# Kernel tuning notes

Measured on AMD Instinct MI355X. Metric: run time of the kernel, lower is better.

## Reference

```python
import jax, jax.numpy as jnp
import numpy as np

BN_EPS = 1e-5
LN_EPS = 1e-5

N_NODES = 50000
N_EDGES = 800000
D_IN = 128
D_HID = 512


def _batchnorm(h, gamma, beta):
    # training-mode BatchNorm1d: biased variance over the node/batch dim
    m = jnp.mean(h, axis=0)
    v = jnp.mean(jnp.square(h - m), axis=0)
    return (h - m) * jax.lax.rsqrt(v + BN_EPS) * gamma + beta


def setup_inputs() -> dict:
    key = jax.random.key(0)
    ks = jax.random.split(key, 8)
    x = jax.random.normal(ks[0], (N_NODES, D_IN), dtype=jnp.float32)
    edge_index = jax.random.randint(ks[1], (2, N_EDGES), 0, N_NODES, dtype=jnp.int64)
    s1 = 1.0 / np.sqrt(D_IN)
    s2 = 1.0 / np.sqrt(D_HID)
    W1 = jax.random.uniform(ks[2], (D_IN, D_HID), jnp.float32, -s1, s1)
    b1 = jax.random.uniform(ks[3], (D_HID,), jnp.float32, -s1, s1)
    W2 = jax.random.uniform(ks[4], (D_HID, D_IN), jnp.float32, -s2, s2)
    b2 = jax.random.uniform(ks[5], (D_IN,), jnp.float32, -s2, s2)
    return {
        "x": x,
        "edge_index": edge_index,
        "W1": W1, "b1": b1,
        "bn1_g": jnp.ones((D_HID,), jnp.float32), "bn1_b": jnp.zeros((D_HID,), jnp.float32),
        "W2": W2, "b2": b2,
        "bn2_g": jnp.ones((D_IN,), jnp.float32), "bn2_b": jnp.zeros((D_IN,), jnp.float32),
        "ln_g": jnp.ones((D_IN,), jnp.float32), "ln_b": jnp.zeros((D_IN,), jnp.float32),
    }


def reference(x, edge_index, W1, b1, bn1_g, bn1_b, W2, b2, bn2_g, bn2_b, ln_g, ln_b):
    n = x.shape[0]
    src = edge_index[0]
    dst = edge_index[1]
    # GIN aggregation: sum of neighbor (source) features at each destination node
    agg = jax.ops.segment_sum(x[src], dst, num_segments=n)  # [N, D_IN]
    h = x + agg  # (1 + eps) * x + agg, eps = 0
    # MLP: Linear -> BN -> ReLU -> Linear -> BN -> ReLU (final activation)
    h = jax.nn.relu(_batchnorm(h @ W1 + b1, bn1_g, bn1_b))  # [N, D_HID]
    h = jax.nn.relu(_batchnorm(h @ W2 + b2, bn2_g, bn2_b))  # [N, D_IN]
    # residual + LayerNorm (dropout p=0 -> identity)
    out = h + x
    m = jnp.mean(out, axis=-1, keepdims=True)
    v = jnp.mean(jnp.square(out - m), axis=-1, keepdims=True)
    out = (out - m) * jax.lax.rsqrt(v + LN_EPS) * ln_g + ln_b
    return out
```

## Files before the change

kernel.cpp:

```cpp
#include <hip/hip_runtime.h>
#include <stdint.h>

#define N_NODES 50000
#define N_EDGES 800000
#define D_IN    128
#define D_HID   512
#define NPAD    50048
#define NTILES  391
#define SCAN_NB 196
#define G_TILES 782
#define G_BLOCKS 256
#define H1_FULL_NEED 64797440LL
#define FILL_CH 2048
#define FILL_SUB ((N_EDGES + FILL_CH - 1) / FILL_CH)

typedef __attribute__((ext_vector_type(8))) short short8;
typedef __attribute__((ext_vector_type(4))) float f32x4;

__device__ __forceinline__ float bf2f(unsigned short u) {
    union { unsigned int i; float f; } v; v.i = ((unsigned int)u) << 16; return v.f;
}
__device__ __forceinline__ unsigned short f2bf(float f) {
    union { float f; unsigned int i; } v; v.f = f;
    unsigned int r = v.i + 0x7fffu + ((v.i >> 16) & 1u);
    return (unsigned short)(r >> 16);
}
__device__ __forceinline__ float loadP(const void* p, long i, int isf) {
    return isf ? ((const float*)p)[i] : bf2f(((const unsigned short*)p)[i]);
}

__global__ void k_init(const void* __restrict__ x, const int* __restrict__ ei,
                       float* __restrict__ stats, int* __restrict__ counts,
                       int* __restrict__ flags) {
    int t = threadIdx.x;
    if (blockIdx.x < 201) {
        int i = blockIdx.x * 256 + t;
        if (i < 1408) stats[i] = 0.f;
        else if (i < 1408 + N_NODES) counts[i - 1408] = 0;
    } else {
        __shared__ int sh[2];
        if (t == 0) { sh[0] = 0; sh[1] = 1; }
        __syncthreads();
        const unsigned short* xu = (const unsigned short*)x;
        for (int i = t; i < 8192; i += 256)
            if (((xu[i] >> 7) & 0xFF) == 0xFF) sh[0] = 1;
        for (int k = t; k < 64; k += 256)
            if (ei[2 * k + 1] != 0) sh[1] = 0;
        __syncthreads();
        if (t == 0) { flags[0] = sh[0]; flags[1] = sh[1]; }
    }
}

__global__ __launch_bounds__(256) void k_prep(const void* __restrict__ W1, const void* __restrict__ W2,
                                              unsigned short* __restrict__ w1t, unsigned short* __restrict__ w2t,
                                              const int* __restrict__ ei, int* __restrict__ counts,
                                              const int* __restrict__ flags) {
    int isf = flags[0];
    if (blockIdx.x < 512) {
        int idx = blockIdx.x * 256 + threadIdx.x;
        if (idx < D_IN * D_HID) {
            int n = idx >> 7, k = idx & 127;
            int src = k * D_HID + n;
            w1t[idx] = isf ? f2bf(((const float*)W1)[src])
                           : ((const unsigned short*)W1)[src];
        } else {
            int j = idx - D_IN * D_HID;
            int n = j >> 9, k = j & 511;
            int src = k * D_IN + n;
            w2t[j] = isf ? f2bf(((const float*)W2)[src])
                         : ((const unsigned short*)W2)[src];
        }
    } else {
        int i64 = flags[1];
        int bid = blockIdx.x - 512;
        int gid = bid & 7;
        int sub = bid >> 3;
        int lo = gid * (N_NODES / 8), hi = lo + (N_NODES / 8);
        int base = sub * FILL_CH + threadIdx.x;
#pragma unroll
        for (int i = 0; i < 8; i++) {
            int e = base + i * 256;
            if (e < N_EDGES) {
                int d = i64 ? ei[2 * N_EDGES + 2 * e] : ei[N_EDGES + e];
                d = min(max(d, 0), N_NODES - 1);
                if (d >= lo && d < hi) atomicAdd(&counts[d], 1);
            }
        }
    }
}

__global__ __launch_bounds__(256) void k_scan_block(const int* __restrict__ counts,
                                                    int* __restrict__ rowptr,
                                                    int* __restrict__ partials) {
    __shared__ int a[256], b[256];
    int t = threadIdx.x;
    int idx = blockIdx.x * 256 + t;
    int c = (idx < N_NODES) ? counts[idx] : 0;
    a[t] = c;
    __syncthreads();
    int* src = a; int* dst = b;
    for (int off = 1; off < 256; off <<= 1) {
        dst[t] = src[t] + ((t >= off) ? src[t - off] : 0);
        __syncthreads();
        int* tmp = src; src = dst; dst = tmp;
    }
    if (idx < N_NODES) rowptr[idx] = src[t] - c;
    if (t == 255) partials[blockIdx.x] = src[255];
}

__global__ __launch_bounds__(256) void k_scan_add(int* __restrict__ rowptr, int* __restrict__ cursor,
                                                  const int* __restrict__ partials) {
    __shared__ int red[256];
    int t = threadIdx.x, bid = blockIdx.x;
    red[t] = (t < SCAN_NB && t < bid) ? partials[t] : 0;
    __syncthreads();
#pragma unroll
    for (int off = 128; off > 0; off >>= 1) {
        if (t < off) red[t] += red[t + off];
        __syncthreads();
    }
    int prefix = red[0];
    int idx = bid * 256 + t;
    if (idx < N_NODES) {
        int v = rowptr[idx] + prefix;
        rowptr[idx] = v;
        cursor[idx] = v;
    } else if (idx == N_NODES) {
        rowptr[N_NODES] = N_EDGES;
    }
}

__global__ __launch_bounds__(256) void k_fill(const int* __restrict__ ei, int* __restrict__ cursor,
                                              int* __restrict__ bucket, const int* __restrict__ flags) {
    int i64 = flags[1];
    int gid = blockIdx.x & 7;
    int sub = blockIdx.x >> 3;
    int lo = gid * (N_NODES / 8), hi = lo + (N_NODES / 8);
    int base = sub * FILL_CH + threadIdx.x;
#pragma unroll
    for (int i = 0; i < 8; i++) {
        int e = base + i * 256;
        if (e < N_EDGES) {
            int d = i64 ? ei[2 * N_EDGES + 2 * e] : ei[N_EDGES + e];
            d = min(max(d, 0), N_NODES - 1);
            if (d >= lo && d < hi) {
                int s = i64 ? ei[2 * e] : ei[e];
                s = min(max(s, 0), N_NODES - 1);
                int pos = atomicAdd(&cursor[d], 1);
                bucket[pos] = s;
            }
        }
    }
}

__global__ __launch_bounds__(256) void k_gather(const int* __restrict__ rowptr,
                                                const int* __restrict__ bucket,
                                                const void* __restrict__ x,
                                                unsigned short* __restrict__ agg,
                                                const int* __restrict__ flags) {
    int isf = flags[0];
    int w = threadIdx.x >> 6, lane = threadIdx.x & 63;
    int row = blockIdx.x * 4 + w;
    float a0 = 0.f, a1 = 0.f;
    if (row < N_NODES) {
        int beg = rowptr[row], end = rowptr[row + 1];
        if (isf) {
            const float* xf = (const float*)x;
            float2 v = *(const float2*)(xf + (size_t)row * D_IN + lane * 2);
            a0 = v.x; a1 = v.y;
            int j = beg;
            for (; j + 8 <= end; j += 8) {
                float2 n0 = *(const float2*)(xf + (size_t)bucket[j] * D_IN + lane * 2);
                float2 n1 = *(const float2*)(xf + (size_t)bucket[j + 1] * D_IN + lane * 2);
                float2 n2 = *(const float2*)(xf + (size_t)bucket[j + 2] * D_IN + lane * 2);
                float2 n3 = *(const float2*)(xf + (size_t)bucket[j + 3] * D_IN + lane * 2);
                float2 n4 = *(const float2*)(xf + (size_t)bucket[j + 4] * D_IN + lane * 2);
                float2 n5 = *(const float2*)(xf + (size_t)bucket[j + 5] * D_IN + lane * 2);
                float2 n6 = *(const float2*)(xf + (size_t)bucket[j + 6] * D_IN + lane * 2);
                float2 n7 = *(const float2*)(xf + (size_t)bucket[j + 7] * D_IN + lane * 2);
                a0 += ((n0.x + n1.x) + (n2.x + n3.x)) + ((n4.x + n5.x) + (n6.x + n7.x));
                a1 += ((n0.y + n1.y) + (n2.y + n3.y)) + ((n4.y + n5.y) + (n6.y + n7.y));
            }
            for (; j + 4 <= end; j += 4) {
                float2 n0 = *(const float2*)(xf + (size_t)bucket[j] * D_IN + lane * 2);
                float2 n1 = *(const float2*)(xf + (size_t)bucket[j + 1] * D_IN + lane * 2);
                float2 n2 = *(const float2*)(xf + (size_t)bucket[j + 2] * D_IN + lane * 2);
                float2 n3 = *(const float2*)(xf + (size_t)bucket[j + 3] * D_IN + lane * 2);
                a0 += (n0.x + n1.x) + (n2.x + n3.x);
                a1 += (n0.y + n1.y) + (n2.y + n3.y);
            }
            for (; j < end; j++) {
                float2 n = *(const float2*)(xf + (size_t)bucket[j] * D_IN + lane * 2);
                a0 += n.x; a1 += n.y;
            }
        } else {
            const unsigned int* xu = (const unsigned int*)x;
            unsigned int u = xu[(size_t)row * 64 + lane];
            a0 = bf2f(u & 0xffff); a1 = bf2f(u >> 16);
            int j = beg;
            for (; j + 8 <= end; j += 8) {
                unsigned int u0 = xu[(size_t)bucket[j] * 64 + lane];
                unsigned int u1 = xu[(size_t)bucket[j + 1] * 64 + lane];
                unsigned int u2 = xu[(size_t)bucket[j + 2] * 64 + lane];
                unsigned int u3 = xu[(size_t)bucket[j + 3] * 64 + lane];
                unsigned int u4 = xu[(size_t)bucket[j + 4] * 64 + lane];
                unsigned int u5 = xu[(size_t)bucket[j + 5] * 64 + lane];
                unsigned int u6 = xu[(size_t)bucket[j + 6] * 64 + lane];
                unsigned int u7 = xu[(size_t)bucket[j + 7] * 64 + lane];
                a0 += ((bf2f(u0 & 0xffff) + bf2f(u1 & 0xffff)) + (bf2f(u2 & 0xffff) + bf2f(u3 & 0xffff)))
                    + ((bf2f(u4 & 0xffff) + bf2f(u5 & 0xffff)) + (bf2f(u6 & 0xffff) + bf2f(u7 & 0xffff)));
                a1 += ((bf2f(u0 >> 16) + bf2f(u1 >> 16)) + (bf2f(u2 >> 16) + bf2f(u3 >> 16)))
                    + ((bf2f(u4 >> 16) + bf2f(u5 >> 16)) + (bf2f(u6 >> 16) + bf2f(u7 >> 16)));
            }
            for (; j + 4 <= end; j += 4) {
                unsigned int u0 = xu[(size_t)bucket[j] * 64 + lane];
                unsigned int u1 = xu[(size_t)bucket[j + 1] * 64 + lane];
                unsigned int u2 = xu[(size_t)bucket[j + 2] * 64 + lane];
                unsigned int u3 = xu[(size_t)bucket[j + 3] * 64 + lane];
                a0 += (bf2f(u0 & 0xffff) + bf2f(u1 & 0xffff)) + (bf2f(u2 & 0xffff) + bf2f(u3 & 0xffff));
                a1 += (bf2f(u0 >> 16) + bf2f(u1 >> 16)) + (bf2f(u2 >> 16) + bf2f(u3 >> 16));
            }
            for (; j < end; j++) {
                unsigned int n = xu[(size_t)bucket[j] * 64 + lane];
                a0 += bf2f(n & 0xffff); a1 += bf2f(n >> 16);
            }
        }
    }
    unsigned int o = (unsigned int)f2bf(a0) | ((unsigned int)f2bf(a1) << 16);
    ((unsigned int*)agg)[(size_t)row * 64 + lane] = o;
}

__global__ __launch_bounds__(256) void k_gram(const unsigned short* __restrict__ aggb,
                                              float* __restrict__ Gpart,
                                              float* __restrict__ colsum) {
    __shared__ unsigned short ldsT[128 * 64];
    int t = threadIdx.x;
    int wid = t >> 6, lane = t & 63;
    int wm = wid & 1, wn = wid >> 1;
    int quad = lane >> 4, l16 = lane & 15;
    f32x4 acc[4][4] = {};
    float cs = 0.f;
    int cscol = t & 127, cskh = t >> 7;
    for (int tile = blockIdx.x; tile < G_TILES; tile += G_BLOCKS) {
        __syncthreads();
        size_t rowbase = (size_t)tile * 64;
#pragma unroll
        for (int jj = 0; jj < 2; jj++) {
            int j = t + jj * 256;
            int c = j >> 5, rp = j & 31;
            uint4 v0 = *(const uint4*)(aggb + (rowbase + 2 * rp) * 128 + c * 8);
            uint4 v1 = *(const uint4*)(aggb + (rowbase + 2 * rp + 1) * 128 + c * 8);
            const unsigned short* p0 = (const unsigned short*)&v0;
            const unsigned short* p1 = (const unsigned short*)&v1;
            int k = 2 * rp, kc = k >> 3, ko = k & 7;
#pragma unroll
            for (int e = 0; e < 8; e++) {
                int col = c * 8 + e;
                *(unsigned int*)(ldsT + col * 64 + ((kc ^ (col & 7)) * 8) + ko) =
                    (unsigned int)p0[e] | ((unsigned int)p1[e] << 16);
            }
        }
        __syncthreads();
#pragma unroll
        for (int ksub = 0; ksub < 2; ksub++) {
            short8 fa[4], fb[4];
#pragma unroll
            for (int mt = 0; mt < 4; mt++) {
                int col = wm * 64 + mt * 16 + l16;
                fa[mt] = *(const short8*)(ldsT + col * 64 + (((ksub * 4 + quad) ^ (col & 7)) * 8));
            }
#pragma unroll
            for (int nt = 0; nt < 4; nt++) {
                int col = wn * 64 + nt * 16 + l16;
                fb[nt] = *(const short8*)(ldsT + col * 64 + (((ksub * 4 + quad) ^ (col & 7)) * 8));
            }
#pragma unroll
            for (int mt = 0; mt < 4; mt++)
#pragma unroll
                for (int nt = 0; nt < 4; nt++)
                    acc[mt][nt] = __builtin_amdgcn_mfma_f32_16x16x32_bf16(fa[mt], fb[nt], acc[mt][nt], 0, 0, 0);
        }
#pragma unroll
        for (int kc = 0; kc < 4; kc++) {
            short8 v = *(const short8*)(ldsT + cscol * 64 + (((cskh * 4 + kc) ^ (cscol & 7)) * 8));
#pragma unroll
            for (int e = 0; e < 8; e++) cs += bf2f((unsigned short)v[e]);
        }
    }
    float* gp = Gpart + (size_t)blockIdx.x * 16384;
#pragma unroll
    for (int mt = 0; mt < 4; mt++)
#pragma unroll
        for (int nt = 0; nt < 4; nt++) {
            int m = wm * 64 + mt * 16 + quad * 4;
            int n = wn * 64 + nt * 16 + l16;
#pragma unroll
            for (int rg = 0; rg < 4; rg++)
                gp[(m + rg) * 128 + n] = acc[mt][nt][rg];
        }
    atomicAdd(&colsum[cscol], cs);
}

__global__ void k_gred(const float* __restrict__ Gpart, float* __restrict__ G) {
    int i = blockIdx.x * 256 + threadIdx.x;
    float s = 0.f;
#pragma unroll 8
    for (int b = 0; b < G_BLOCKS; b++) s += Gpart[(size_t)b * 16384 + i];
    G[i] = s;
}

__global__ __launch_bounds__(256) void k_bn1(const float* __restrict__ G,
                                             const float* __restrict__ colsum,
                                             const unsigned short* __restrict__ w1t,
                                             const void* __restrict__ b1,
                                             float* __restrict__ sum1,
                                             float* __restrict__ sumsq1,
                                             const int* __restrict__ flags) {
    int isf = flags[0];
    __shared__ float wsh[4][128];
    int t = threadIdx.x, wid = t >> 6, lane = t & 63;
    int n = blockIdx.x * 4 + wid;
    unsigned int u = *(const unsigned int*)(w1t + (size_t)n * 128 + lane * 2);
    wsh[wid][lane * 2] = bf2f(u & 0xffff);
    wsh[wid][lane * 2 + 1] = bf2f(u >> 16);
    __syncthreads();
    const float* w = wsh[wid];
    const f32x4* g0 = (const f32x4*)(G + (size_t)lane * 128);
    const f32x4* g1 = (const f32x4*)(G + (size_t)(lane + 64) * 128);
    float t0 = 0.f, t1 = 0.f;
#pragma unroll 4
    for (int q4 = 0; q4 < 32; q4++) {
        f32x4 a = g0[q4], b = g1[q4];
        float w0 = w[q4 * 4], w1 = w[q4 * 4 + 1], w2 = w[q4 * 4 + 2], w3 = w[q4 * 4 + 3];
        t0 += a[0] * w0 + a[1] * w1 + a[2] * w2 + a[3] * w3;
        t1 += b[0] * w0 + b[1] * w1 + b[2] * w2 + b[3] * w3;
    }
    float sq = w[lane] * t0 + w[lane + 64] * t1;
    float s  = w[lane] * colsum[lane] + w[lane + 64] * colsum[lane + 64];
#pragma unroll
    for (int m = 1; m < 64; m <<= 1) {
        sq += __shfl_xor(sq, m, 64);
        s  += __shfl_xor(s, m, 64);
    }
    if (lane == 0) {
        float b = loadP(b1, n, isf);
        sum1[n]   = s + (float)N_NODES * b;
        sumsq1[n] = sq + 2.f * b * s + (float)N_NODES * b * b;
    }
}

__global__ __launch_bounds__(256, 2) void k_mlp1(const unsigned short* __restrict__ aggc,
                                                 const unsigned short* __restrict__ w1t,
                                                 const void* __restrict__ b1,
                                                 const void* __restrict__ g1,
                                                 const void* __restrict__ bb1,
                                                 const float* __restrict__ sum1,
                                                 const float* __restrict__ sumsq1,
                                                 unsigned short* __restrict__ h1c,
                                                 const int* __restrict__ flags) {
    __shared__ unsigned short bufA[128 * 128];
    __shared__ unsigned short bufW[128 * 128];
    int isf = flags[0];
    int t = threadIdx.x;
    int m0 = (blockIdx.x >> 2) * 128;
    int nb = blockIdx.x & 3;
    int r = t >> 1, half = t & 1;
    int wid = t >> 6, lane = t & 63;
    int wm = wid & 1, wn = wid >> 1;
    int quad = lane >> 4, l16 = lane & 15;
#pragma unroll
    for (int i = 0; i < 8; i++) {
        int chunk = half * 8 + i;
        int sw = ((chunk ^ (r & 15)) * 8);
        *(uint4*)(bufA + r * 128 + sw) = *(const uint4*)(aggc + (size_t)(m0 + r) * 128 + chunk * 8);
        *(uint4*)(bufW + r * 128 + sw) = *(const uint4*)(w1t + (size_t)(nb * 128 + r) * 128 + chunk * 8);
    }
    __syncthreads();
    f32x4 acc[4][4] = {};
#pragma unroll
    for (int ks = 0; ks < 4; ks++) {
        short8 af[4], bw[4];
#pragma unroll
        for (int mt = 0; mt < 4; mt++)
            af[mt] = *(const short8*)(bufA + (wm * 64 + mt * 16 + l16) * 128 + (((ks * 4 + quad) ^ l16) * 8));
#pragma unroll
        for (int nt = 0; nt < 4; nt++)
            bw[nt] = *(const short8*)(bufW + (wn * 64 + nt * 16 + l16) * 128 + (((ks * 4 + quad) ^ l16) * 8));
#pragma unroll
        for (int mt = 0; mt < 4; mt++)
#pragma unroll
            for (int nt = 0; nt < 4; nt++)
                acc[mt][nt] = __builtin_amdgcn_mfma_f32_16x16x32_bf16(af[mt], bw[nt], acc[mt][nt], 0, 0, 0);
    }
    __syncthreads();
#pragma unroll
    for (int nt = 0; nt < 4; nt++) {
        int nl = wn * 64 + nt * 16 + l16;
        int n1 = nb * 128 + nl;
        float mz = sum1[n1] * (1.f / N_NODES);
        float vz = sumsq1[n1] * (1.f / N_NODES) - mz * mz;
        float inv = rsqrtf(fmaxf(vz, 0.f) + 1e-5f);
        float A = loadP(g1, n1, isf) * inv;
        float C = loadP(bb1, n1, isf) - mz * A + loadP(b1, n1, isf) * A;
        int ccw = nl >> 3, cl = nl & 7;
#pragma unroll
        for (int mt = 0; mt < 4; mt++)
#pragma unroll
            for (int rg = 0; rg < 4; rg++) {
                int R = wm * 64 + mt * 16 + quad * 4 + rg;
                bufA[R * 128 + ((ccw ^ (R & 15)) * 8) + cl] = f2bf(fmaxf(acc[mt][nt][rg] * A + C, 0.f));
            }
    }
    __syncthreads();
#pragma unroll
    for (int i = 0; i < 8; i++) {
        int idx = t + i * 256;
        int rr = idx >> 4, chunk = idx & 15;
        *(uint4*)(h1c + (size_t)(m0 + rr) * D_HID + nb * 128 + chunk * 8) =
            *(const uint4*)(bufA + rr * 128 + ((chunk ^ (rr & 15)) * 8));
    }
}

__global__ __launch_bounds__(256, 2) void k_mlp1r(const unsigned short* __restrict__ aggb,
                                                  const unsigned short* __restrict__ w1t,
                                                  const void* __restrict__ b1,
                                                  unsigned short* __restrict__ h1,
                                                  float* __restrict__ sum1,
                                                  float* __restrict__ sumsq1,
                                                  const int* __restrict__ flags) {
    __shared__ unsigned short bufA[128 * 128];
    __shared__ unsigned short bufW[128 * 128];
    __shared__ float sred[256];
    int isf = flags[0];
    int t = threadIdx.x;
    int m0 = (blockIdx.x >> 2) * 128;
    int nb = blockIdx.x & 3;
    int r = t >> 1, half = t & 1;
    int wid = t >> 6, lane = t & 63;
    int wm = wid & 1, wn = wid >> 1;
    int quad = lane >> 4, l16 = lane & 15;
    sred[t] = 0.f;
#pragma unroll
    for (int i = 0; i < 8; i++) {
        int chunk = half * 8 + i;
        int sw = ((chunk ^ (r & 15)) * 8);
        *(uint4*)(bufA + r * 128 + sw) = *(const uint4*)(aggb + (size_t)(m0 + r) * 128 + chunk * 8);
        *(uint4*)(bufW + r * 128 + sw) = *(const uint4*)(w1t + (size_t)(nb * 128 + r) * 128 + chunk * 8);
    }
    __syncthreads();
    f32x4 acc[4][4] = {};
#pragma unroll
    for (int ks = 0; ks < 4; ks++) {
        short8 af[4], bw[4];
#pragma unroll
        for (int mt = 0; mt < 4; mt++)
            af[mt] = *(const short8*)(bufA + (wm * 64 + mt * 16 + l16) * 128 + (((ks * 4 + quad) ^ l16) * 8));
#pragma unroll
        for (int nt = 0; nt < 4; nt++)
            bw[nt] = *(const short8*)(bufW + (wn * 64 + nt * 16 + l16) * 128 + (((ks * 4 + quad) ^ l16) * 8));
#pragma unroll
        for (int mt = 0; mt < 4; mt++)
#pragma unroll
            for (int nt = 0; nt < 4; nt++)
                acc[mt][nt] = __builtin_amdgcn_mfma_f32_16x16x32_bf16(af[mt], bw[nt], acc[mt][nt], 0, 0, 0);
    }
    __syncthreads();
#pragma unroll
    for (int nt = 0; nt < 4; nt++) {
        int nl = wn * 64 + nt * 16 + l16;
        int n1 = nb * 128 + nl;
        float bias = loadP(b1, n1, isf);
        int ccw = nl >> 3, cl = nl & 7;
        float s = 0.f, ss = 0.f;
#pragma unroll
        for (int mt = 0; mt < 4; mt++)
#pragma unroll
            for (int rg = 0; rg < 4; rg++) {
                int R = wm * 64 + mt * 16 + quad * 4 + rg;
                float z = acc[mt][nt][rg] + bias;
                bufA[R * 128 + ((ccw ^ (R & 15)) * 8) + cl] = f2bf(z);
                if (m0 + R < N_NODES) { s += z; ss += z * z; }
            }
        s += __shfl_xor(s, 16, 64); ss += __shfl_xor(ss, 16, 64);
        s += __shfl_xor(s, 32, 64); ss += __shfl_xor(ss, 32, 64);
        if (quad == 0) { atomicAdd(&sred[nl], s); atomicAdd(&sred[128 + nl], ss); }
    }
    __syncthreads();
#pragma unroll
    for (int i = 0; i < 8; i++) {
        int idx = t + i * 256;
        int rr = idx >> 4, chunk = idx & 15;
        *(uint4*)(h1 + (size_t)(m0 + rr) * D_HID + nb * 128 + chunk * 8) =
            *(const uint4*)(bufA + rr * 128 + ((chunk ^ (rr & 15)) * 8));
    }
    if (t < 128)      atomicAdd(&sum1[nb * 128 + t], sred[t]);
    else              atomicAdd(&sumsq1[nb * 128 + (t - 128)], sred[t]);
}

__global__ __launch_bounds__(256, 3) void k_mlp2(const unsigned short* __restrict__ h1c,
                                                 const unsigned short* __restrict__ w2t,
                                                 const void* __restrict__ b2,
                                                 unsigned short* __restrict__ h2c,
                                                 float* __restrict__ sum2,
                                                 float* __restrict__ sumsq2,
                                                 const int* __restrict__ flags,
                                                 int roff) {
    __shared__ unsigned short bufA[64 * 128];
    __shared__ unsigned short bufW[128 * 128];
    __shared__ float sred[256];
    int isf = flags[0];
    int t = threadIdx.x;
    int m0 = blockIdx.x * 64;
    int rw = t >> 1, halfw = t & 1;
    int wid = t >> 6, lane = t & 63;
    int wm = wid & 1, wn = wid >> 1;
    int quad = lane >> 4, l16 = lane & 15;
    sred[t] = 0.f;
    f32x4 acc[2][4] = {};
    for (int kb = 0; kb < 4; kb++) {
        __syncthreads();
#pragma unroll
        for (int i = 0; i < 4; i++) {
            int idx = t + i * 256;
            int rr = idx >> 4, chunk = idx & 15;
            *(uint4*)(bufA + rr * 128 + ((chunk ^ (rr & 15)) * 8)) =
                *(const uint4*)(h1c + (size_t)(m0 + rr) * D_HID + kb * 128 + chunk * 8);
        }
#pragma unroll
        for (int i = 0; i < 8; i++) {
            int chunk = halfw * 8 + i;
            *(uint4*)(bufW + rw * 128 + ((chunk ^ (rw & 15)) * 8)) =
                *(const uint4*)(w2t + (size_t)rw * D_HID + kb * 128 + chunk * 8);
        }
        __syncthreads();
#pragma unroll
        for (int ks = 0; ks < 4; ks++) {
            short8 af[2], bw[4];
#pragma unroll
            for (int mt = 0; mt < 2; mt++)
                af[mt] = *(const short8*)(bufA + (wm * 32 + mt * 16 + l16) * 128 + (((ks * 4 + quad) ^ l16) * 8));
#pragma unroll
            for (int nt = 0; nt < 4; nt++)
                bw[nt] = *(const short8*)(bufW + (wn * 64 + nt * 16 + l16) * 128 + (((ks * 4 + quad) ^ l16) * 8));
#pragma unroll
            for (int mt = 0; mt < 2; mt++)
#pragma unroll
                for (int nt = 0; nt < 4; nt++)
                    acc[mt][nt] = __builtin_amdgcn_mfma_f32_16x16x32_bf16(af[mt], bw[nt], acc[mt][nt], 0, 0, 0);
        }
    }
    __syncthreads();
#pragma unroll
    for (int nt = 0; nt < 4; nt++) {
        int n = wn * 64 + nt * 16 + l16;
        float bias = loadP(b2, n, isf);
        float s = 0.f, ss = 0.f;
#pragma unroll
        for (int mt = 0; mt < 2; mt++) {
            int Rl = wm * 32 + mt * 16 + quad * 4;
#pragma unroll
            for (int rg = 0; rg < 4; rg++) {
                float z = acc[mt][nt][rg] + bias;
                bufW[(Rl + rg) * 128 + n] = f2bf(z);
                if (roff + m0 + Rl + rg < N_NODES) { s += z; ss += z * z; }
            }
        }
        s += __shfl_xor(s, 16, 64); ss += __shfl_xor(ss, 16, 64);
        s += __shfl_xor(s, 32, 64); ss += __shfl_xor(ss, 32, 64);
        if (quad == 0) { atomicAdd(&sred[n], s); atomicAdd(&sred[128 + n], ss); }
    }
    __syncthreads();
#pragma unroll
    for (int i = 0; i < 4; i++) {
        int idx = t + i * 256;
        int rr = idx >> 4, seg = idx & 15;
        *(uint4*)(h2c + (size_t)(m0 + rr) * D_IN + seg * 8) = *(const uint4*)(bufW + rr * 128 + seg * 8);
    }
    {
        int n = t & 127;
        if (t < 128) atomicAdd(&sum2[n], sred[n]);
        else         atomicAdd(&sumsq2[n], sred[128 + n]);
    }
}

__global__ __launch_bounds__(512, 4) void k_mlp2b(const unsigned short* __restrict__ h1,
                                                  const unsigned short* __restrict__ w2t,
                                                  const void* __restrict__ b2,
                                                  const void* __restrict__ g1,
                                                  const void* __restrict__ bb1,
                                                  const float* __restrict__ sum1,
                                                  const float* __restrict__ sumsq1,
                                                  unsigned short* __restrict__ h2,
                                                  float* __restrict__ sum2,
                                                  float* __restrict__ sumsq2,
                                                  const int* __restrict__ flags) {
    __shared__ unsigned short bufA[128 * 128];
    __shared__ unsigned short bufW[128 * 128];
    __shared__ float sred[256];
    __shared__ __align__(16) float bnA[512];
    __shared__ __align__(16) float bnC[512];
    int isf = flags[0];
    int t = threadIdx.x;
    int m0 = blockIdx.x * 128;
    int wid = t >> 6, lane = t & 63;
    int wm = wid & 3, wn = wid >> 2;
    int quad = lane >> 4, l16 = lane & 15;
    int chunkT = t & 15;
    if (t < 256) sred[t] = 0.f;
    if (t < 512) {
        float mz = sum1[t] * (1.f / N_NODES);
        float vz = sumsq1[t] * (1.f / N_NODES) - mz * mz;
        float inv = rsqrtf(fmaxf(vz, 0.f) + 1e-5f);
        float A = loadP(g1, t, isf) * inv;
        bnA[t] = A;
        bnC[t] = loadP(bb1, t, isf) - mz * A;
    }
    f32x4 acc[2][4] = {};
    for (int kb = 0; kb < 4; kb++) {
        __syncthreads();
        f32x4 A0 = *(const f32x4*)(bnA + kb * 128 + chunkT * 8);
        f32x4 A1 = *(const f32x4*)(bnA + kb * 128 + chunkT * 8 + 4);
        f32x4 C0 = *(const f32x4*)(bnC + kb * 128 + chunkT * 8);
        f32x4 C1 = *(const f32x4*)(bnC + kb * 128 + chunkT * 8 + 4);
#pragma unroll
        for (int i = 0; i < 4; i++) {
            int idx = t + i * 512;
            int rr = idx >> 4;
            uint4 v = *(const uint4*)(h1 + (size_t)(m0 + rr) * D_HID + kb * 128 + chunkT * 8);
            const unsigned short* pv = (const unsigned short*)&v;
            unsigned short o[8];
            o[0] = f2bf(fmaxf(bf2f(pv[0]) * A0[0] + C0[0], 0.f));
            o[1] = f2bf(fmaxf(bf2f(pv[1]) * A0[1] + C0[1], 0.f));
            o[2] = f2bf(fmaxf(bf2f(pv[2]) * A0[2] + C0[2], 0.f));
            o[3] = f2bf(fmaxf(bf2f(pv[3]) * A0[3] + C0[3], 0.f));
            o[4] = f2bf(fmaxf(bf2f(pv[4]) * A1[0] + C1[0], 0.f));
            o[5] = f2bf(fmaxf(bf2f(pv[5]) * A1[1] + C1[1], 0.f));
            o[6] = f2bf(fmaxf(bf2f(pv[6]) * A1[2] + C1[2], 0.f));
            o[7] = f2bf(fmaxf(bf2f(pv[7]) * A1[3] + C1[3], 0.f));
            *(uint4*)(bufA + rr * 128 + ((chunkT ^ (rr & 15)) * 8)) = *(const uint4*)o;
        }
#pragma unroll
        for (int i = 0; i < 4; i++) {
            int idx = t + i * 512;
            int rr = idx >> 4;
            *(uint4*)(bufW + rr * 128 + ((chunkT ^ (rr & 15)) * 8)) =
                *(const uint4*)(w2t + (size_t)rr * D_HID + kb * 128 + chunkT * 8);
        }
        __syncthreads();
#pragma unroll
        for (int ks = 0; ks < 4; ks++) {
            short8 af[2], bw[4];
#pragma unroll
            for (int mt = 0; mt < 2; mt++)
                af[mt] = *(const short8*)(bufA + (wm * 32 + mt * 16 + l16) * 128 + (((ks * 4 + quad) ^ l16) * 8));
#pragma unroll
            for (int nt = 0; nt < 4; nt++)
                bw[nt] = *(const short8*)(bufW + (wn * 64 + nt * 16 + l16) * 128 + (((ks * 4 + quad) ^ l16) * 8));
#pragma unroll
            for (int mt = 0; mt < 2; mt++)
#pragma unroll
                for (int nt = 0; nt < 4; nt++)
                    acc[mt][nt] = __builtin_amdgcn_mfma_f32_16x16x32_bf16(af[mt], bw[nt], acc[mt][nt], 0, 0, 0);
        }
    }
    __syncthreads();
#pragma unroll
    for (int nt = 0; nt < 4; nt++) {
        int n = wn * 64 + nt * 16 + l16;
        float bias = loadP(b2, n, isf);
        float s = 0.f, ss = 0.f;
#pragma unroll
        for (int mt = 0; mt < 2; mt++) {
            int Rl = wm * 32 + mt * 16 + quad * 4;
#pragma unroll
            for (int rg = 0; rg < 4; rg++) {
                float z = acc[mt][nt][rg] + bias;
                bufW[(Rl + rg) * 128 + n] = f2bf(z);
                if (m0 + Rl + rg < N_NODES) { s += z; ss += z * z; }
            }
        }
        s += __shfl_xor(s, 16, 64); ss += __shfl_xor(ss, 16, 64);
        s += __shfl_xor(s, 32, 64); ss += __shfl_xor(ss, 32, 64);
        if (quad == 0) { atomicAdd(&sred[n], s); atomicAdd(&sred[128 + n], ss); }
    }
    __syncthreads();
#pragma unroll
    for (int i = 0; i < 4; i++) {
        int idx = t + i * 512;
        int rr = idx >> 4, seg = idx & 15;
        *(uint4*)(h2 + (size_t)(m0 + rr) * D_IN + seg * 8) = *(const uint4*)(bufW + rr * 128 + seg * 8);
    }
    if (t < 256) {
        int n = t & 127;
        if (t < 128) atomicAdd(&sum2[n], sred[n]);
        else         atomicAdd(&sumsq2[n], sred[128 + n]);
    }
}

__global__ __launch_bounds__(256) void k_final(const unsigned short* __restrict__ h2,
                                               const void* __restrict__ x,
                                               const float* __restrict__ sum2,
                                               const float* __restrict__ sumsq2,
                                               const void* __restrict__ g2,
                                               const void* __restrict__ bb2,
                                               const void* __restrict__ lng,
                                               const void* __restrict__ lnb,
                                               void* __restrict__ out,
                                               const int* __restrict__ flags) {
    int isf = flags[0];
    __shared__ float a2s[D_IN], c2s[D_IN];
    int t = threadIdx.x;
    if (t < D_IN) {
        float m = sum2[t] * (1.f / N_NODES);
        float v = sumsq2[t] * (1.f / N_NODES) - m * m;
        float inv = rsqrtf(fmaxf(v, 0.f) + 1e-5f);
        float a = loadP(g2, t, isf) * inv;
        a2s[t] = a;
        c2s[t] = loadP(bb2, t, isf) - m * a;
    }
    __syncthreads();
    int w = t >> 6, lane = t & 63;
    int row = blockIdx.x * 4 + w;
    if (row >= N_NODES) return;
    size_t base = (size_t)row * D_IN;
    int c0 = lane * 2, c1 = lane * 2 + 1;
    unsigned int hu = ((const unsigned int*)h2)[base / 2 + lane];
    float x0, x1;
    if (isf) {
        float2 xv = *((const float2*)x + base / 2 + lane);
        x0 = xv.x; x1 = xv.y;
    } else {
        unsigned int xu = ((const unsigned int*)x)[base / 2 + lane];
        x0 = bf2f(xu & 0xffff); x1 = bf2f(xu >> 16);
    }
    float o0 = fmaxf(a2s[c0] * bf2f(hu & 0xffff) + c2s[c0], 0.f) + x0;
    float o1 = fmaxf(a2s[c1] * bf2f(hu >> 16) + c2s[c1], 0.f) + x1;
    float s = o0 + o1, ss = o0 * o0 + o1 * o1;
#pragma unroll
    for (int m = 1; m < 64; m <<= 1) {
        s += __shfl_xor(s, m, 64);
        ss += __shfl_xor(ss, m, 64);
    }
    float mean = s * (1.f / D_IN);
    float var = ss * (1.f / D_IN) - mean * mean;
    float inv = rsqrtf(fmaxf(var, 0.f) + 1e-5f);
    float r0 = (o0 - mean) * inv * loadP(lng, c0, isf) + loadP(lnb, c0, isf);
    float r1 = (o1 - mean) * inv * loadP(lng, c1, isf) + loadP(lnb, c1, isf);
    if (isf) {
        *((float2*)out + base / 2 + lane) = make_float2(r0, r1);
    } else {
        ((unsigned int*)out)[base / 2 + lane] = (unsigned int)f2bf(r0) | ((unsigned int)f2bf(r1) << 16);
    }
}

extern "C" void kernel_launch(void* const* d_in, const int* in_sizes, int n_in,
                              void* d_out, int out_size, void* d_ws, size_t ws_size,
                              hipStream_t stream) {
    const void* x    = d_in[0];
    const int*  ei   = (const int*)d_in[1];
    const void* W1   = d_in[2];
    const void* b1   = d_in[3];
    const void* bn1g = d_in[4];
    const void* bn1b = d_in[5];
    const void* W2   = d_in[6];
    const void* b2   = d_in[7];
    const void* bn2g = d_in[8];
    const void* bn2b = d_in[9];
    const void* lng  = d_in[10];
    const void* lnb  = d_in[11];

    char* ws = (char*)d_ws;
    float* stats   = (float*)ws;
    float* sum1    = stats;
    float* sumsq1  = stats + 512;
    float* sum2    = stats + 1024;
    float* sumsq2  = stats + 1152;
    float* colsum  = stats + 1280;
    int*   flags   = (int*)(ws + 5632);
    int*   partials= (int*)(ws + 5696);
    int*   rowptr  = (int*)(ws + 8192);
    int*   cursor  = (int*)(ws + 208256);
    unsigned short* w1t = (unsigned short*)(ws + 408320);
    unsigned short* w2t = (unsigned short*)(ws + 539392);
    float* G       = (float*)(ws + 670464);
    unsigned short* agg = (unsigned short*)(ws + 736000);
    unsigned short* h2  = agg;
    int*   bucket  = (int*)(ws + 13548288);
    float* Gpart   = (float*)(ws + 16748288);
    unsigned short* h1r = (unsigned short*)(ws + 13548288);

    k_init<<<202, 256, 0, stream>>>(x, ei, stats, cursor, flags);
    k_prep<<<512 + 8 * FILL_SUB, 256, 0, stream>>>(W1, W2, w1t, w2t, ei, cursor, flags);
    k_scan_block<<<SCAN_NB, 256, 0, stream>>>(cursor, rowptr, partials);
    k_scan_add<<<SCAN_NB, 256, 0, stream>>>(rowptr, cursor, partials);
    k_fill<<<8 * FILL_SUB, 256, 0, stream>>>(ei, cursor, bucket, flags);
    k_gather<<<NPAD / 4, 256, 0, stream>>>(rowptr, bucket, x, agg, flags);

    if ((long long)ws_size >= H1_FULL_NEED) {
        k_mlp1r<<<NTILES * 4, 256, 0, stream>>>(agg, w1t, b1, h1r, sum1, sumsq1, flags);
        k_mlp2b<<<NTILES, 512, 0, stream>>>(h1r, w2t, b2, bn1g, bn1b, sum1, sumsq1,
                                            h2, sum2, sumsq2, flags);
    } else {
        k_gram<<<G_BLOCKS, 256, 0, stream>>>(agg, Gpart, colsum);
        k_gred<<<64, 256, 0, stream>>>(Gpart, G);
        k_bn1<<<128, 256, 0, stream>>>(G, colsum, w1t, b1, sum1, sumsq1, flags);
        long long avail = (long long)ws_size - 13548288LL;
        int max_tiles = (avail > 0) ? (int)(avail / 131072LL) : 1;
        if (max_tiles < 1)  max_tiles = 1;
        if (max_tiles > NTILES) max_tiles = NTILES;
        int nch = (NTILES + max_tiles - 1) / max_tiles;
        int per = (NTILES + nch - 1) / nch;
        for (int done = 0; done < NTILES; done += per) {
            int nt = NTILES - done;
            if (nt > per) nt = per;
            const unsigned short* aggc = agg + (size_t)done * 128 * 128;
            unsigned short* h2c = h2 + (size_t)done * 128 * 128;
            k_mlp1<<<nt * 4, 256, 0, stream>>>(aggc, w1t, b1, bn1g, bn1b, sum1, sumsq1, h1r, flags);
            k_mlp2<<<nt * 2, 256, 0, stream>>>(h1r, w2t, b2, h2c, sum2, sumsq2, flags, done * 128);
        }
    }

    k_final<<<(N_NODES + 3) / 4, 256, 0, stream>>>(h2, x, sum2, sumsq2, bn2g, bn2b, lng, lnb, d_out, flags);
}
```

Measured before the change: 324.5 us.

## Fuse neighbor gather into first MLP GEMM kernel with LDS staging

Adds a kernel that performs the CSR neighbor aggregation for a 128-row tile directly into shared memory, then multiplies by W1 with MFMA and writes h1 plus BN1 statistics. This removes the separate gather launch and the global write/read of the aggregated tensor when the workspace is large enough. The trade-off is fewer, larger blocks doing the latency-bound gather serially per wave, and high LDS use that limits occupancy.

```diff
diff --git a/kernel.cpp b/kernel.cpp
--- a/kernel.cpp
+++ b/kernel.cpp
@@ -10,7 +10,8 @@
 #define SCAN_NB 196
 #define G_TILES 782
 #define G_BLOCKS 256
-#define H1_FULL_NEED 64797440LL
+#define H1_SEP_NEED   64797440LL
+#define H1_FUSED_NEED 67997440LL
 #define FILL_CH 2048
 #define FILL_SUB ((N_EDGES + FILL_CH - 1) / FILL_CH)
 
@@ -228,6 +229,162 @@
     }
     unsigned int o = (unsigned int)f2bf(a0) | ((unsigned int)f2bf(a1) << 16);
     ((unsigned int*)agg)[(size_t)row * 64 + lane] = o;
+}
+
+__global__ __launch_bounds__(512, 4) void k_gmlp1(const int* __restrict__ rowptr,
+                                                  const int* __restrict__ bucket,
+                                                  const void* __restrict__ x,
+                                                  const unsigned short* __restrict__ w1t,
+                                                  const void* __restrict__ b1,
+                                                  unsigned short* __restrict__ h1,
+                                                  float* __restrict__ sum1,
+                                                  float* __restrict__ sumsq1,
+                                                  const int* __restrict__ flags) {
+    __shared__ unsigned short bufA[128 * 128];
+    __shared__ unsigned short bufW[128 * 128];
+    __shared__ float sred[256];
+    int isf = flags[0];
+    int t = threadIdx.x;
+    int m0 = blockIdx.x * 128;
+    int w8 = t >> 6, lane = t & 63;
+    if (t < 256) sred[t] = 0.f;
+    for (int rl = 0; rl < 16; rl++) {
+        int r = w8 * 16 + rl;
+        int row = m0 + r;
+        float a0 = 0.f, a1 = 0.f;
+        if (row < N_NODES) {
+            int beg = rowptr[row], end = rowptr[row + 1];
+            if (isf) {
+                const float* xf = (const float*)x;
+                float2 v = *(const float2*)(xf + (size_t)row * D_IN + lane * 2);
+                a0 = v.x; a1 = v.y;
+                int j = beg;
+                for (; j + 8 <= end; j += 8) {
+                    float2 n0 = *(const float2*)(xf + (size_t)bucket[j] * D_IN + lane * 2);
+                    float2 n1 = *(const float2*)(xf + (size_t)bucket[j + 1] * D_IN + lane * 2);
+                    float2 n2 = *(const float2*)(xf + (size_t)bucket[j + 2] * D_IN + lane * 2);
+                    float2 n3 = *(const float2*)(xf + (size_t)bucket[j + 3] * D_IN + lane * 2);
+                    float2 n4 = *(const float2*)(xf + (size_t)bucket[j + 4] * D_IN + lane * 2);
+                    float2 n5 = *(const float2*)(xf + (size_t)bucket[j + 5] * D_IN + lane * 2);
+                    float2 n6 = *(const float2*)(xf + (size_t)bucket[j + 6] * D_IN + lane * 2);
+                    float2 n7 = *(const float2*)(xf + (size_t)bucket[j + 7] * D_IN + lane * 2);
+                    a0 += ((n0.x + n1.x) + (n2.x + n3.x)) + ((n4.x + n5.x) + (n6.x + n7.x));
+                    a1 += ((n0.y + n1.y) + (n2.y + n3.y)) + ((n4.y + n5.y) + (n6.y + n7.y));
+                }
+                for (; j + 4 <= end; j += 4) {
+                    float2 n0 = *(const float2*)(xf + (size_t)bucket[j] * D_IN + lane * 2);
+                    float2 n1 = *(const float2*)(xf + (size_t)bucket[j + 1] * D_IN + lane * 2);
+                    float2 n2 = *(const float2*)(xf + (size_t)bucket[j + 2] * D_IN + lane * 2);
+                    float2 n3 = *(const float2*)(xf + (size_t)bucket[j + 3] * D_IN + lane * 2);
+                    a0 += (n0.x + n1.x) + (n2.x + n3.x);
+                    a1 += (n0.y + n1.y) + (n2.y + n3.y);
+                }
+                for (; j < end; j++) {
+                    float2 n = *(const float2*)(xf + (size_t)bucket[j] * D_IN + lane * 2);
+                    a0 += n.x; a1 += n.y;
+                }
+            } else {
+                const unsigned int* xu = (const unsigned int*)x;
+                unsigned int u = xu[(size_t)row * 64 + lane];
+                a0 = bf2f(u & 0xffff); a1 = bf2f(u >> 16);
+                int j = beg;
+                for (; j + 8 <= end; j += 8) {
+                    unsigned int u0 = xu[(size_t)bucket[j] * 64 + lane];
+                    unsigned int u1 = xu[(size_t)bucket[j + 1] * 64 + lane];
+                    unsigned int u2 = xu[(size_t)bucket[j + 2] * 64 + lane];
+                    unsigned int u3 = xu[(size_t)bucket[j + 3] * 64 + lane];
+                    unsigned int u4 = xu[(size_t)bucket[j + 4] * 64 + lane];
+                    unsigned int u5 = xu[(size_t)bucket[j + 5] * 64 + lane];
+                    unsigned int u6 = xu[(size_t)bucket[j + 6] * 64 + lane];
+                    unsigned int u7 = xu[(size_t)bucket[j + 7] * 64 + lane];
+                    a0 += ((bf2f(u0 & 0xffff) + bf2f(u1 & 0xffff)) + (bf2f(u2 & 0xffff) + bf2f(u3 & 0xffff)))
+                        + ((bf2f(u4 & 0xffff) + bf2f(u5 & 0xffff)) + (bf2f(u6 & 0xffff) + bf2f(u7 & 0xffff)));
+                    a1 += ((bf2f(u0 >> 16) + bf2f(u1 >> 16)) + (bf2f(u2 >> 16) + bf2f(u3 >> 16)))
+                        + ((bf2f(u4 >> 16) + bf2f(u5 >> 16)) + (bf2f(u6 >> 16) + bf2f(u7 >> 16)));
+                }
+                for (; j + 4 <= end; j += 4) {
+                    unsigned int u0 = xu[(size_t)bucket[j] * 64 + lane];
+                    unsigned int u1 = xu[(size_t)bucket[j + 1] * 64 + lane];
+                    unsigned int u2 = xu[(size_t)bucket[j + 2] * 64 + lane];
+                    unsigned int u3 = xu[(size_t)bucket[j + 3] * 64 + lane];
+                    a0 += (bf2f(u0 & 0xffff) + bf2f(u1 & 0xffff)) + (bf2f(u2 & 0xffff) + bf2f(u3 & 0xffff));
+                    a1 += (bf2f(u0 >> 16) + bf2f(u1 >> 16)) + (bf2f(u2 >> 16) + bf2f(u3 >> 16));
+                }
+                for (; j < end; j++) {
+                    unsigned int n = xu[(size_t)bucket[j] * 64 + lane];
+                    a0 += bf2f(n & 0xffff); a1 += bf2f(n >> 16);
+                }
+            }
+        }
+        int c = lane * 2, chunk = c >> 3, off = c & 7;
+        *(unsigned int*)(bufA + r * 128 + ((chunk ^ (r & 15)) * 8) + off) =
+            (unsigned int)f2bf(a0) | ((unsigned int)f2bf(a1) << 16);
+    }
+    int wid = t >> 6;
+    int wm = wid & 3, wn = wid >> 2;
+    int quad = lane >> 4, l16 = lane & 15;
+    for (int nb = 0; nb < 4; nb++) {
+#pragma unroll
+        for (int i = 0; i < 4; i++) {
+            int idx = t + i * 512;
+            int rr = idx >> 4, chunk = idx & 15;
+            *(uint4*)(bufW + rr * 128 + ((chunk ^ (rr & 15)) * 8)) =
+                *(const uint4*)(w1t + (size_t)(nb * 128 + rr) * 128 + chunk * 8);
+        }
+        __syncthreads();
+        f32x4 acc[2][4] = {};
+#pragma unroll
+        for (int ks = 0; ks < 4; ks++) {
+            short8 af[2], bw[4];
+#pragma unroll
+            for (int mt = 0; mt < 2; mt++)
+                af[mt] = *(const short8*)(bufA + (wm * 32 + mt * 16 + l16) * 128 + (((ks * 4 + quad) ^ l16) * 8));
+#pragma unroll
+            for (int nt = 0; nt < 4; nt++)
+                bw[nt] = *(const short8*)(bufW + (wn * 64 + nt * 16 + l16) * 128 + (((ks * 4 + quad) ^ l16) * 8));
+#pragma unroll
+            for (int mt = 0; mt < 2; mt++)
+#pragma unroll
+                for (int nt = 0; nt < 4; nt++)
+                    acc[mt][nt] = __builtin_amdgcn_mfma_f32_16x16x32_bf16(af[mt], bw[nt], acc[mt][nt], 0, 0, 0);
+        }
+        __syncthreads();
+#pragma unroll
+        for (int nt = 0; nt < 4; nt++) {
+            int n = wn * 64 + nt * 16 + l16;
+            int n1 = nb * 128 + n;
+            float bias = loadP(b1, n1, isf);
+            float s = 0.f, ss = 0.f;
+#pragma unroll
+            for (int mt = 0; mt < 2; mt++) {
+#pragma unroll
+                for (int rg = 0; rg < 4; rg++) {
+                    int Rl = wm * 32 + mt * 16 + quad * 4 + rg;
+                    float z = acc[mt][nt][rg] + bias;
+                    bufW[Rl * 128 + n] = f2bf(z);
+                    if (m0 + Rl < N_NODES) { s += z; ss += z * z; }
+                }
+            }
+            s += __shfl_xor(s, 16, 64); ss += __shfl_xor(ss, 16, 64);
+            s += __shfl_xor(s, 32, 64); ss += __shfl_xor(ss, 32, 64);
+            if (quad == 0) { atomicAdd(&sred[n], s); atomicAdd(&sred[128 + n], ss); }
+        }
+        __syncthreads();
+#pragma unroll
+        for (int i = 0; i < 4; i++) {
+            int idx = t + i * 512;
+            int rr = idx >> 4, seg = idx & 15;
+            *(uint4*)(h1 + (size_t)(m0 + rr) * D_HID + nb * 128 + seg * 8) =
+                *(const uint4*)(bufW + rr * 128 + seg * 8);
+        }
+        if (t < 256) {
+            int n = t & 127;
+            if (t < 128) atomicAdd(&sum1[nb * 128 + n], sred[n]);
+            else         atomicAdd(&sumsq1[nb * 128 + n], sred[128 + n]);
+            sred[t] = 0.f;
+        }
+        __syncthreads();
+    }
 }
 
 __global__ __launch_bounds__(256) void k_gram(const unsigned short* __restrict__ aggb,
@@ -787,20 +944,26 @@
     unsigned short* h2  = agg;
     int*   bucket  = (int*)(ws + 13548288);
     float* Gpart   = (float*)(ws + 16748288);
-    unsigned short* h1r = (unsigned short*)(ws + 13548288);
+    unsigned short* h1sep  = (unsigned short*)(ws + 13548288);
+    unsigned short* h1fuse = (unsigned short*)(ws + 16748288);
 
     k_init<<<202, 256, 0, stream>>>(x, ei, stats, cursor, flags);
     k_prep<<<512 + 8 * FILL_SUB, 256, 0, stream>>>(W1, W2, w1t, w2t, ei, cursor, flags);
     k_scan_block<<<SCAN_NB, 256, 0, stream>>>(cursor, rowptr, partials);
     k_scan_add<<<SCAN_NB, 256, 0, stream>>>(rowptr, cursor, partials);
     k_fill<<<8 * FILL_SUB, 256, 0, stream>>>(ei, cursor, bucket, flags);
-    k_gather<<<NPAD / 4, 256, 0, stream>>>(rowptr, bucket, x, agg, flags);
-
-    if ((long long)ws_size >= H1_FULL_NEED) {
-        k_mlp1r<<<NTILES * 4, 256, 0, stream>>>(agg, w1t, b1, h1r, sum1, sumsq1, flags);
-        k_mlp2b<<<NTILES, 512, 0, stream>>>(h1r, w2t, b2, bn1g, bn1b, sum1, sumsq1,
+
+    if ((long long)ws_size >= H1_FUSED_NEED) {
+        k_gmlp1<<<NTILES, 512, 0, stream>>>(rowptr, bucket, x, w1t, b1, h1fuse, sum1, sumsq1, flags);
+        k_mlp2b<<<NTILES, 512, 0, stream>>>(h1fuse, w2t, b2, bn1g, bn1b, sum1, sumsq1,
+                                            h2, sum2, sumsq2, flags);
+    } else if ((long long)ws_size >= H1_SEP_NEED) {
+        k_gather<<<NPAD / 4, 256, 0, stream>>>(rowptr, bucket, x, agg, flags);
+        k_mlp1r<<<NTILES * 4, 256, 0, stream>>>(agg, w1t, b1, h1sep, sum1, sumsq1, flags);
+        k_mlp2b<<<NTILES, 512, 0, stream>>>(h1sep, w2t, b2, bn1g, bn1b, sum1, sumsq1,
                                             h2, sum2, sumsq2, flags);
     } else {
+        k_gather<<<NPAD / 4, 256, 0, stream>>>(rowptr, bucket, x, agg, flags);
         k_gram<<<G_BLOCKS, 256, 0, stream>>>(agg, Gpart, colsum);
         k_gred<<<64, 256, 0, stream>>>(Gpart, G);
         k_bn1<<<128, 256, 0, stream>>>(G, colsum, w1t, b1, sum1, sumsq1, flags);
@@ -815,8 +978,8 @@
             if (nt > per) nt = per;
             const unsigned short* aggc = agg + (size_t)done * 128 * 128;
             unsigned short* h2c = h2 + (size_t)done * 128 * 128;
-            k_mlp1<<<nt * 4, 256, 0, stream>>>(aggc, w1t, b1, bn1g, bn1b, sum1, sumsq1, h1r, flags);
-            k_mlp2<<<nt * 2, 256, 0, stream>>>(h1r, w2t, b2, h2c, sum2, sumsq2, flags, done * 128);
+            k_mlp1<<<nt * 4, 256, 0, stream>>>(aggc, w1t, b1, bn1g, bn1b, sum1, sumsq1, h1sep, flags);
+            k_mlp2<<<nt * 2, 256, 0, stream>>>(h1sep, w2t, b2, h2c, sum2, sumsq2, flags, done * 128);
         }
     }
 
```

After: 319.9 us. Within noise of the previous version (-1.4%).
